# Kernel tuning notes

Hardware: AMD Instinct MI355X
Metric: run time of the kernel (lower is better)

The kernel has to match this reference:

```python
import jax, jax.numpy as jnp
import numpy as np

SEQ, D_A, H, D_K, D_V = 4096, 2048, 16, 128, 128


def setup_inputs() -> dict:
    key = jax.random.key(0)
    ks = jax.random.split(key, 7)
    return {
        "queries": jax.random.normal(ks[0], (SEQ, D_A), dtype=jnp.float32),
        "keys":    jax.random.normal(ks[1], (SEQ, D_A), dtype=jnp.float32),
        "values":  jax.random.normal(ks[2], (SEQ, D_A), dtype=jnp.float32),
        "Eq": jax.random.normal(ks[3], (H, D_A, D_K), dtype=jnp.float32),
        "Ek": jax.random.normal(ks[4], (H, D_A, D_K), dtype=jnp.float32),
        "Ev": jax.random.normal(ks[5], (H, D_A, D_V), dtype=jnp.float32),
        "W_out": jax.random.normal(ks[6], (H * D_V, D_A), dtype=jnp.float32),
    }


def reference(queries, keys, values, Eq, Ek, Ev, W_out):
    # Per-head projections: [seq, d_a] x [h, d_a, d] -> [h, seq, d]
    Q = jnp.einsum("sd,hdk->hsk", queries, Eq)
    K = jnp.einsum("sd,hdk->hsk", keys, Ek)
    V = jnp.einsum("sd,hdv->hsv", values, Ev)
    scale = 1.0 / D_K  # faithful to source: 1/d_k, not 1/sqrt(d_k)
    dots = jnp.einsum("hqk,hsk->hqs", Q, K) * scale  # [h, seq, seq]
    attn = jax.nn.softmax(dots, axis=-1)  # dropout p=0 -> identity
    out = jnp.einsum("hqs,hsv->hqv", attn, V)  # [h, seq, d_v]
    # concat heads along last dim: [seq, h*d_v]
    A = jnp.transpose(out, (1, 0, 2)).reshape(SEQ, H * D_V)
    return A @ W_out  # [seq, d_a]
```

## Files before the change

### kernel.cpp

```cpp
#include <hip/hip_runtime.h>

typedef unsigned short u16;
typedef __attribute__((ext_vector_type(4)))  float  f32x4;
typedef __attribute__((ext_vector_type(16))) float  f32x16;
typedef __attribute__((ext_vector_type(4)))  float  float4v;
typedef __attribute__((ext_vector_type(4)))  unsigned short u16x4;
typedef __attribute__((ext_vector_type(8)))  unsigned short u16x8;
typedef __attribute__((ext_vector_type(8)))  short s16x8;
typedef __attribute__((ext_vector_type(4)))  unsigned int u32x4;

#define SEQ 4096
#define DA  2048
#define NH  16
#define DKV 128

__device__ __forceinline__ u16 f2bf(float f) {
    unsigned u = __builtin_bit_cast(unsigned, f);
    u += 0x7FFFu + ((u >> 16) & 1u);
    return (u16)(u >> 16);
}
__device__ __forceinline__ float bf2f(u16 h) {
    return __builtin_bit_cast(float, (unsigned)h << 16);
}
__device__ __forceinline__ f32x4 mfma16(u16x8 a, u16x8 b, f32x4 c) {
    return __builtin_amdgcn_mfma_f32_16x16x32_bf16(
        __builtin_bit_cast(s16x8, a), __builtin_bit_cast(s16x8, b), c, 0, 0, 0);
}
__device__ __forceinline__ f32x16 mfma32(u16x8 a, u16x8 b, f32x16 c) {
    return __builtin_amdgcn_mfma_f32_32x32x16_bf16(
        __builtin_bit_cast(s16x8, a), __builtin_bit_cast(s16x8, b), c, 0, 0, 0);
}
__device__ __forceinline__ unsigned cvtpk(float lo, float hi) {
    unsigned r;
    asm("v_cvt_pk_bf16_f32 %0, %1, %2" : "=v"(r) : "v"(lo), "v"(hi));
    return r;
}
__device__ __forceinline__ void gld16(const u16* g, u16* l) {
    __builtin_amdgcn_global_load_lds(
        (const __attribute__((address_space(1))) unsigned int*)g,
        (__attribute__((address_space(3))) unsigned int*)l, 16, 0, 0);
}
__device__ __forceinline__ char* ldsp(void* base, int row, int bcol, int rowbytes) {
    int off = row * rowbytes + bcol;
    off ^= (row & 7) << 4;
    return (char*)base + off;
}
__device__ __forceinline__ char* ldsp256(void* base, int row, int bcol) {
    int off = row * 256 + bcol;
    off ^= (row & 15) << 4;
    return (char*)base + off;
}

__global__ void transpose_split_k(const float* __restrict__ in, u16* __restrict__ oh,
                                  u16* __restrict__ ol, int R, int C) {
    __shared__ float tile[32][33];
    int b  = blockIdx.z;
    int r0 = blockIdx.x * 32, c0 = blockIdx.y * 32;
    const float* src = in + (size_t)b * R * C;
    int t = threadIdx.x;
    {
        int cl = t & 31, r = t >> 5;
        for (int i = 0; i < 4; ++i)
            tile[r + 8 * i][cl] = src[(size_t)(r0 + r + 8 * i) * C + (c0 + cl)];
    }
    __syncthreads();
    int rl = t & 31, c = t >> 5;
    size_t obase = (size_t)b * R * C;
    for (int i = 0; i < 4; ++i) {
        int cw = c + 8 * i;
        float x = tile[rl][cw];
        u16 h = f2bf(x);
        size_t o = obase + (size_t)(c0 + cw) * R + (r0 + rl);
        oh[o] = h;
        if (ol) ol[o] = f2bf(x - bf2f(h));
    }
}

template <int MODE>
__global__ void __launch_bounds__(256, 2) proj_k(const float* __restrict__ A,
                                                 const u16* __restrict__ BTh,
                                                 const u16* __restrict__ BTl,
                                                 u16* __restrict__ Oh,
                                                 u16* __restrict__ Ol) {
    __shared__ u16 sAh[128 * 64];
    __shared__ u16 sBh[128 * 64];
    __shared__ u16 sAl[MODE ? 128 * 64 : 8];
    __shared__ u16 sBl[MODE ? 128 * 64 : 8];

    int t = threadIdx.x;
    int h = blockIdx.y;
    int bm0 = blockIdx.x * 128;
    int lane = t & 63, w = t >> 6, wr = w >> 1, wc = w & 1;
    int g = lane >> 4, c = lane & 15;

    f32x4 acc[4][4] = {};

    float4v pA[8];
    u16x8   pBh[4], pBl[4];

    auto prefetch = [&](int k0) {
#pragma unroll
        for (int i = 0; i < 8; ++i) {
            int idx = t + i * 256;
            int row = idx >> 4, c4 = idx & 15;
            pA[i] = *(const float4v*)(A + (size_t)(bm0 + row) * DA + k0 + c4 * 4);
        }
#pragma unroll
        for (int i = 0; i < 4; ++i) {
            int idx = t + i * 256;
            int row = idx >> 3, c8 = idx & 7;
            size_t gb = ((size_t)h * 128 + row) * DA + k0 + c8 * 8;
            pBh[i] = *(const u16x8*)(BTh + gb);
            if (MODE) pBl[i] = *(const u16x8*)(BTl + gb);
        }
    };
    auto write_lds = [&]() {
#pragma unroll
        for (int i = 0; i < 8; ++i) {
            int idx = t + i * 256;
            int row = idx >> 4, c4 = idx & 15;
            u16x4 hv, lv;
#pragma unroll
            for (int j = 0; j < 4; ++j) {
                u16 hh = f2bf(pA[i][j]);
                hv[j] = hh;
                lv[j] = f2bf(pA[i][j] - bf2f(hh));
            }
            *(u16x4*)ldsp(sAh, row, c4 * 8, 128) = hv;
            if (MODE) *(u16x4*)ldsp(sAl, row, c4 * 8, 128) = lv;
        }
#pragma unroll
        for (int i = 0; i < 4; ++i) {
            int idx = t + i * 256;
            int row = idx >> 3, c8 = idx & 7;
            *(u16x8*)ldsp(sBh, row, c8 * 16, 128) = pBh[i];
            if (MODE) *(u16x8*)ldsp(sBl, row, c8 * 16, 128) = pBl[i];
        }
    };

    prefetch(0);
    for (int k0 = 0; k0 < DA; k0 += 64) {
        __syncthreads();
        write_lds();
        __syncthreads();
        int nxt = (k0 + 64 < DA) ? k0 + 64 : 0;
        prefetch(nxt);

        for (int kc = 0; kc < 2; ++kc) {
            int kb = (kc * 32 + g * 8) * 2;
            u16x8 ah[4], al[4], bh[4], bl[4];
            for (int m = 0; m < 4; ++m) {
                int row = wr * 64 + m * 16 + c;
                ah[m] = *(u16x8*)ldsp(sAh, row, kb, 128);
                if (MODE) al[m] = *(u16x8*)ldsp(sAl, row, kb, 128);
            }
            for (int n = 0; n < 4; ++n) {
                int row = wc * 64 + n * 16 + c;
                bh[n] = *(u16x8*)ldsp(sBh, row, kb, 128);
                if (MODE) bl[n] = *(u16x8*)ldsp(sBl, row, kb, 128);
            }
            for (int m = 0; m < 4; ++m)
                for (int n = 0; n < 4; ++n) {
                    acc[m][n] = mfma16(ah[m], bh[n], acc[m][n]);
                    if (MODE) {
                        acc[m][n] = mfma16(ah[m], bl[n], acc[m][n]);
                        acc[m][n] = mfma16(al[m], bh[n], acc[m][n]);
                    }
                }
        }
    }

    const float scale = (MODE == 2) ? (1.0f / 128.0f) : 1.0f;
    for (int m = 0; m < 4; ++m)
        for (int n = 0; n < 4; ++n) {
            int col  = wc * 64 + n * 16 + c;
            int row0 = bm0 + wr * 64 + m * 16 + g * 4;
            if (MODE == 0) {
                u16x4 pv;
                for (int j = 0; j < 4; ++j) pv[j] = f2bf(acc[m][n][j]);
                *(u16x4*)(Oh + ((size_t)h * DKV + col) * SEQ + row0) = pv;
            } else {
                for (int j = 0; j < 4; ++j) {
                    float v = acc[m][n][j] * scale;
                    u16 hh = f2bf(v);
                    size_t o = ((size_t)h * SEQ + row0 + j) * DKV + col;
                    Oh[o] = hh;
                    Ol[o] = f2bf(v - bf2f(hh));
                }
            }
        }
}

__global__ void __launch_bounds__(256, 2) attn_k(const u16* __restrict__ QH,
                                                 const u16* __restrict__ QL,
                                                 const u16* __restrict__ KH,
                                                 const u16* __restrict__ KL,
                                                 const u16* __restrict__ VT,
                                                 u16* __restrict__ Abuf) {
    __shared__ u16 sKh[64 * 128];
    __shared__ u16 sKl[64 * 128];
    __shared__ u16 sV[64 * 128];

    int t = threadIdx.x, lane = t & 63, w = t >> 6;
    int h = blockIdx.y, q0 = blockIdx.x * 128;
    int c = lane & 31, hi = lane >> 5;
    int qrow = q0 + w * 32 + c;

    u16x8 qh[8], ql[8];
    {
        size_t base = ((size_t)h * SEQ + qrow) * DKV + hi * 8;
#pragma unroll
        for (int dc = 0; dc < 8; ++dc) {
            qh[dc] = *(const u16x8*)(QH + base + dc * 16);
            ql[dc] = *(const u16x8*)(QL + base + dc * 16);
        }
    }

    f32x16 o[4] = {};
    float mrun = -3e38f, lrun = 0.f;

    const size_t kroot = (size_t)h * SEQ * DKV;
    const size_t vroot = (size_t)h * DKV * SEQ;

    for (int kv0 = 0; kv0 < SEQ; kv0 += 64) {
        __syncthreads();
        {
            const u16* khp = KH + kroot + (size_t)kv0 * DKV;
            const u16* klp = KL + kroot + (size_t)kv0 * DKV;
            const u16* vtp = VT + vroot + kv0;
#pragma unroll
            for (int j = 0; j < 4; ++j) {
                int ci = w * 4 + j;
                int rK = ci * 4 + (lane >> 4);
                int cK = (lane & 15) ^ (rK & 15);
                gld16(khp + rK * DKV + cK * 8, &sKh[ci * 512]);
                gld16(klp + rK * DKV + cK * 8, &sKl[ci * 512]);
                int vd = ((cK >> 3) << 6) + rK;
                gld16(vtp + (size_t)vd * SEQ + (cK & 7) * 8, &sV[ci * 512]);
            }
        }
        __syncthreads();

        f32x16 s[2] = {};
        __builtin_amdgcn_s_setprio(1);
#pragma unroll
        for (int kt = 0; kt < 2; ++kt) {
#pragma unroll
            for (int dc = 0; dc < 8; ++dc) {
                u16x8 kh = *(u16x8*)ldsp256(sKh, kt * 32 + c, dc * 32 + hi * 16);
                u16x8 kl = *(u16x8*)ldsp256(sKl, kt * 32 + c, dc * 32 + hi * 16);
                s[kt] = mfma32(kh, qh[dc], s[kt]);
                s[kt] = mfma32(kl, qh[dc], s[kt]);
                s[kt] = mfma32(kh, ql[dc], s[kt]);
            }
        }
        __builtin_amdgcn_s_setprio(0);

        float vmax = s[0][0];
#pragma unroll
        for (int r = 1; r < 16; ++r) vmax = fmaxf(vmax, s[0][r]);
#pragma unroll
        for (int r = 0; r < 16; ++r) vmax = fmaxf(vmax, s[1][r]);
        vmax = fmaxf(vmax, __shfl_xor(vmax, 32));
        float mnew = fmaxf(mrun, vmax);
        float corr = __expf(mrun - mnew);
        mrun = mnew;
        float rs = 0.f;
#pragma unroll
        for (int kt = 0; kt < 2; ++kt)
#pragma unroll
            for (int r = 0; r < 16; ++r) {
                float p = __expf(s[kt][r] - mnew);
                s[kt][r] = p;
                rs += p;
            }
        rs += __shfl_xor(rs, 32);
        lrun = lrun * corr + rs;
#pragma unroll
        for (int vt = 0; vt < 4; ++vt)
#pragma unroll
            for (int r = 0; r < 16; ++r) o[vt][r] *= corr;

#pragma unroll
        for (int kt = 0; kt < 2; ++kt) {
            unsigned wv[8], xw[8];
#pragma unroll
            for (int i = 0; i < 8; ++i) wv[i] = cvtpk(s[kt][2 * i], s[kt][2 * i + 1]);
#pragma unroll
            for (int i = 0; i < 8; ++i) xw[i] = (unsigned)__shfl_xor((int)wv[i], 32);
            __builtin_amdgcn_s_setprio(1);
#pragma unroll
            for (int kc = 0; kc < 2; ++kc) {
                u32x4 pw;
                pw[0] = hi ? xw[4 * kc + 2] : wv[4 * kc + 0];
                pw[1] = hi ? xw[4 * kc + 3] : wv[4 * kc + 1];
                pw[2] = hi ? wv[4 * kc + 2] : xw[4 * kc + 0];
                pw[3] = hi ? wv[4 * kc + 3] : xw[4 * kc + 1];
                u16x8 pf = __builtin_bit_cast(u16x8, pw);
#pragma unroll
                for (int vt = 0; vt < 4; ++vt) {
                    int v = vt * 32 + c;
                    u16x8 vf = *(u16x8*)ldsp256(sV, v & 63,
                                                ((v >> 6) << 7) + kt * 64 + kc * 32 + hi * 16);
                    o[vt] = mfma32(vf, pf, o[vt]);
                }
            }
            __builtin_amdgcn_s_setprio(0);
        }
    }

    float inv = 1.0f / lrun;
#pragma unroll
    for (int vt = 0; vt < 4; ++vt)
#pragma unroll
        for (int rg = 0; rg < 4; ++rg) {
            u16x4 pv;
#pragma unroll
            for (int j = 0; j < 4; ++j) pv[j] = f2bf(o[vt][rg * 4 + j] * inv);
            *(u16x4*)(Abuf + (size_t)qrow * (NH * DKV) + h * DKV + vt * 32 + rg * 8 + hi * 4) = pv;
        }
}

__global__ void __launch_bounds__(256, 2) gemm_out_k(const u16* __restrict__ Abuf,
                                                     const u16* __restrict__ WT,
                                                     float* __restrict__ out) {
    __shared__ u16 sA[128 * 64];
    __shared__ u16 sB[128 * 64];
    int t = threadIdx.x, lane = t & 63, w = t >> 6, wr = w >> 1, wc = w & 1;
    int g = lane >> 4, c = lane & 15;
    int bm0 = blockIdx.x * 128, bn0 = blockIdx.y * 128;
    f32x4 acc[4][4] = {};

    u16x8 pA[4], pB[4];
    auto prefetch = [&](int k0) {
#pragma unroll
        for (int i = 0; i < 4; ++i) {
            int idx = t + i * 256, row = idx >> 3, c8 = idx & 7;
            pA[i] = *(const u16x8*)(Abuf + (size_t)(bm0 + row) * DA + k0 + c8 * 8);
            pB[i] = *(const u16x8*)(WT + (size_t)(bn0 + row) * DA + k0 + c8 * 8);
        }
    };
    auto write_lds = [&]() {
#pragma unroll
        for (int i = 0; i < 4; ++i) {
            int idx = t + i * 256, row = idx >> 3, c8 = idx & 7;
            *(u16x8*)ldsp(sA, row, c8 * 16, 128) = pA[i];
            *(u16x8*)ldsp(sB, row, c8 * 16, 128) = pB[i];
        }
    };

    prefetch(0);
    for (int k0 = 0; k0 < DA; k0 += 64) {
        __syncthreads();
        write_lds();
        __syncthreads();
        int nxt = (k0 + 64 < DA) ? k0 + 64 : 0;
        prefetch(nxt);

        for (int kc = 0; kc < 2; ++kc) {
            int kb = (kc * 32 + g * 8) * 2;
            u16x8 af[4], bfq[4];
            for (int m = 0; m < 4; ++m) af[m]  = *(u16x8*)ldsp(sA, wr * 64 + m * 16 + c, kb, 128);
            for (int n = 0; n < 4; ++n) bfq[n] = *(u16x8*)ldsp(sB, wc * 64 + n * 16 + c, kb, 128);
            for (int m = 0; m < 4; ++m)
                for (int n = 0; n < 4; ++n)
                    acc[m][n] = mfma16(af[m], bfq[n], acc[m][n]);
        }
    }
    for (int m = 0; m < 4; ++m)
        for (int n = 0; n < 4; ++n) {
            int row0 = bm0 + wr * 64 + m * 16 + g * 4;
            int col  = bn0 + wc * 64 + n * 16 + c;
            for (int j = 0; j < 4; ++j)
                out[(size_t)(row0 + j) * DA + col] = acc[m][n][j];
        }
}

extern "C" void kernel_launch(void* const* d_in, const int* in_sizes, int n_in,
                              void* d_out, int out_size, void* d_ws, size_t ws_size,
                              hipStream_t stream) {
    const float* queries = (const float*)d_in[0];
    const float* keys    = (const float*)d_in[1];
    const float* values  = (const float*)d_in[2];
    const float* Eq      = (const float*)d_in[3];
    const float* Ek      = (const float*)d_in[4];
    const float* Ev      = (const float*)d_in[5];
    const float* Wout    = (const float*)d_in[6];
    float* out = (float*)d_out;

    const size_t PROJ = (size_t)NH * SEQ * DKV;
    const size_t TSZ  = (size_t)DA * DA;
    u16* p  = (u16*)d_ws;
    u16* QH = p; p += PROJ;
    u16* QL = p; p += PROJ;
    u16* KH = p; p += PROJ;
    u16* KL = p; p += PROJ;
    u16* VT = p; p += PROJ;
    u16* AB = p; p += (size_t)SEQ * NH * DKV;
    u16* TH = p; p += TSZ;
    u16* TL = p; p += TSZ;

    dim3 tgE(DA / 32, DKV / 32, NH);
    dim3 tgW(DA / 32, DA / 32, 1);
    dim3 pg(SEQ / 128, NH);

    transpose_split_k<<<tgE, 256, 0, stream>>>(Eq, TH, TL, DA, DKV);
    proj_k<2><<<pg, 256, 0, stream>>>(queries, TH, TL, QH, QL);
    transpose_split_k<<<tgE, 256, 0, stream>>>(Ek, TH, TL, DA, DKV);
    proj_k<1><<<pg, 256, 0, stream>>>(keys, TH, TL, KH, KL);
    transpose_split_k<<<tgE, 256, 0, stream>>>(Ev, TH, nullptr, DA, DKV);
    proj_k<0><<<pg, 256, 0, stream>>>(values, TH, nullptr, VT, nullptr);
    transpose_split_k<<<tgW, 256, 0, stream>>>(Wout, TH, nullptr, DA, DA);
    attn_k<<<dim3(SEQ / 128, NH), 256, 0, stream>>>(QH, QL, KH, KL, VT, AB);
    gemm_out_k<<<dim3(SEQ / 128, DA / 128), 256, 0, stream>>>(AB, TH, out);
}
```

Measured before the change: 631.6 us.

## Double-buffer attention KV tiles and skip softmax rescale when max barely changes

The attention kernel now uses 512-thread blocks covering 256 query rows, with a flattened grid that interleaves heads across neighbouring blocks. K-high, K-low and V tiles are double-buffered in LDS, so the next tile's loads are issued before the current tile is computed and each iteration needs only one barrier. The online softmax rescales the accumulators and running sum only when some lane's new max exceeds the stored max by more than 8, which removes most per-tile rescale multiplies. The costs are twice the LDS per block, one block per CU instead of two, and possibly larger intermediate exponentials, which stay bounded.

```diff
diff --git a/kernel.cpp b/kernel.cpp
--- a/kernel.cpp
+++ b/kernel.cpp
@@ -191,18 +191,20 @@
         }
 }
 
-__global__ void __launch_bounds__(256, 2) attn_k(const u16* __restrict__ QH,
+__global__ void __launch_bounds__(512, 1) attn_k(const u16* __restrict__ QH,
                                                  const u16* __restrict__ QL,
                                                  const u16* __restrict__ KH,
                                                  const u16* __restrict__ KL,
                                                  const u16* __restrict__ VT,
                                                  u16* __restrict__ Abuf) {
-    __shared__ u16 sKh[64 * 128];
-    __shared__ u16 sKl[64 * 128];
-    __shared__ u16 sV[64 * 128];
+    __shared__ u16 sKh[2][64 * 128];
+    __shared__ u16 sKl[2][64 * 128];
+    __shared__ u16 sV [2][64 * 128];
 
     int t = threadIdx.x, lane = t & 63, w = t >> 6;
-    int h = blockIdx.y, q0 = blockIdx.x * 128;
+    int bid = blockIdx.x;
+    int h  = (bid & 7) + 8 * ((bid >> 3) & 1);
+    int q0 = (bid >> 4) * 256;
     int c = lane & 31, hi = lane >> 5;
     int qrow = q0 + w * 32 + c;
 
@@ -222,24 +224,28 @@
     const size_t kroot = (size_t)h * SEQ * DKV;
     const size_t vroot = (size_t)h * DKV * SEQ;
 
-    for (int kv0 = 0; kv0 < SEQ; kv0 += 64) {
+    auto stage = [&](int kv, int b) {
+        const u16* khp = KH + kroot + (size_t)kv * DKV;
+        const u16* klp = KL + kroot + (size_t)kv * DKV;
+        const u16* vtp = VT + vroot + kv;
+#pragma unroll
+        for (int j = 0; j < 2; ++j) {
+            int ci = w * 2 + j;
+            int rK = ci * 4 + (lane >> 4);
+            int cK = (lane & 15) ^ (rK & 15);
+            gld16(khp + rK * DKV + cK * 8, &sKh[b][ci * 512]);
+            gld16(klp + rK * DKV + cK * 8, &sKl[b][ci * 512]);
+            int vd = ((cK >> 3) << 6) + rK;
+            gld16(vtp + (size_t)vd * SEQ + (cK & 7) * 8, &sV[b][ci * 512]);
+        }
+    };
+
+    stage(0, 0);
+    const int NT = SEQ / 64;
+    for (int it = 0; it < NT; ++it) {
+        int b = it & 1;
         __syncthreads();
-        {
-            const u16* khp = KH + kroot + (size_t)kv0 * DKV;
-            const u16* klp = KL + kroot + (size_t)kv0 * DKV;
-            const u16* vtp = VT + vroot + kv0;
-#pragma unroll
-            for (int j = 0; j < 4; ++j) {
-                int ci = w * 4 + j;
-                int rK = ci * 4 + (lane >> 4);
-                int cK = (lane & 15) ^ (rK & 15);
-                gld16(khp + rK * DKV + cK * 8, &sKh[ci * 512]);
-                gld16(klp + rK * DKV + cK * 8, &sKl[ci * 512]);
-                int vd = ((cK >> 3) << 6) + rK;
-                gld16(vtp + (size_t)vd * SEQ + (cK & 7) * 8, &sV[ci * 512]);
-            }
-        }
-        __syncthreads();
+        if (it + 1 < NT) stage((it + 1) * 64, b ^ 1);
 
         f32x16 s[2] = {};
         __builtin_amdgcn_s_setprio(1);
@@ -247,8 +253,8 @@
         for (int kt = 0; kt < 2; ++kt) {
 #pragma unroll
             for (int dc = 0; dc < 8; ++dc) {
-                u16x8 kh = *(u16x8*)ldsp256(sKh, kt * 32 + c, dc * 32 + hi * 16);
-                u16x8 kl = *(u16x8*)ldsp256(sKl, kt * 32 + c, dc * 32 + hi * 16);
+                u16x8 kh = *(u16x8*)ldsp256(sKh[b], kt * 32 + c, dc * 32 + hi * 16);
+                u16x8 kl = *(u16x8*)ldsp256(sKl[b], kt * 32 + c, dc * 32 + hi * 16);
                 s[kt] = mfma32(kh, qh[dc], s[kt]);
                 s[kt] = mfma32(kl, qh[dc], s[kt]);
                 s[kt] = mfma32(kh, ql[dc], s[kt]);
@@ -262,24 +268,27 @@
 #pragma unroll
         for (int r = 0; r < 16; ++r) vmax = fmaxf(vmax, s[1][r]);
         vmax = fmaxf(vmax, __shfl_xor(vmax, 32));
-        float mnew = fmaxf(mrun, vmax);
-        float corr = __expf(mrun - mnew);
-        mrun = mnew;
+        if (!__all(vmax <= mrun + 8.0f)) {
+            float mnew = fmaxf(mrun, vmax);
+            float corr = __expf(mrun - mnew);
+            mrun = mnew;
+            lrun *= corr;
+#pragma unroll
+            for (int vt = 0; vt < 4; ++vt)
+#pragma unroll
+                for (int r = 0; r < 16; ++r) o[vt][r] *= corr;
+        }
         float rs = 0.f;
 #pragma unroll
         for (int kt = 0; kt < 2; ++kt)
 #pragma unroll
             for (int r = 0; r < 16; ++r) {
-                float p = __expf(s[kt][r] - mnew);
+                float p = __expf(s[kt][r] - mrun);
                 s[kt][r] = p;
                 rs += p;
             }
         rs += __shfl_xor(rs, 32);
-        lrun = lrun * corr + rs;
-#pragma unroll
-        for (int vt = 0; vt < 4; ++vt)
-#pragma unroll
-            for (int r = 0; r < 16; ++r) o[vt][r] *= corr;
+        lrun += rs;
 
 #pragma unroll
         for (int kt = 0; kt < 2; ++kt) {
@@ -300,7 +309,7 @@
 #pragma unroll
                 for (int vt = 0; vt < 4; ++vt) {
                     int v = vt * 32 + c;
-                    u16x8 vf = *(u16x8*)ldsp256(sV, v & 63,
+                    u16x8 vf = *(u16x8*)ldsp256(sV[b], v & 63,
                                                 ((v >> 6) << 7) + kt * 64 + kc * 32 + hi * 16);
                     o[vt] = mfma32(vf, pf, o[vt]);
                 }
@@ -411,6 +420,6 @@
     transpose_split_k<<<tgE, 256, 0, stream>>>(Ev, TH, nullptr, DA, DKV);
     proj_k<0><<<pg, 256, 0, stream>>>(values, TH, nullptr, VT, nullptr);
     transpose_split_k<<<tgW, 256, 0, stream>>>(Wout, TH, nullptr, DA, DA);
-    attn_k<<<dim3(SEQ / 128, NH), 256, 0, stream>>>(QH, QL, KH, KL, VT, AB);
+    attn_k<<<dim3(SEQ / 256 * NH), 512, 0, stream>>>(QH, QL, KH, KL, VT, AB);
     gemm_out_k<<<dim3(SEQ / 128, DA / 128), 256, 0, stream>>>(AB, TH, out);
 }
```

New measurement: 590.6 us, median of 2. -6.5%, faster.
